# Performance work log

Measured on AMD Instinct MI355X. Metric: run time of the kernel, lower is better.

The kernel has to match this reference:

```python
import jax, jax.numpy as jnp
import numpy as np

D_MODEL = 1024
N_HEADS = 16
D_FF = 4096
EPS = 1e-5


def setup_inputs() -> dict:
    key = jax.random.key(0)
    ks = jax.random.split(key, 13)
    d, f = D_MODEL, D_FF
    s = 1.0 / np.sqrt(d)
    sf = 1.0 / np.sqrt(f)
    return {
        "x": jax.random.normal(ks[0], (2, 2048, d), dtype=jnp.float32),
        "Wq": jax.random.normal(ks[1], (d, d), dtype=jnp.float32) * s,
        "bq": jnp.zeros((d,), jnp.float32),
        "Wk": jax.random.normal(ks[2], (d, d), dtype=jnp.float32) * s,
        "bk": jnp.zeros((d,), jnp.float32),
        "Wv": jax.random.normal(ks[3], (d, d), dtype=jnp.float32) * s,
        "bv": jnp.zeros((d,), jnp.float32),
        "Wo": jax.random.normal(ks[4], (d, d), dtype=jnp.float32) * s,
        "bo": jnp.zeros((d,), jnp.float32),
        "W1": jax.random.normal(ks[5], (f, d), dtype=jnp.float32) * s,
        "b1": jnp.zeros((f,), jnp.float32),
        "W2": jax.random.normal(ks[6], (d, f), dtype=jnp.float32) * sf,
        "b2": jnp.zeros((d,), jnp.float32),
        "g1": jnp.ones((d,), jnp.float32),
        "be1": jnp.zeros((d,), jnp.float32),
        "g2": jnp.ones((d,), jnp.float32),
        "be2": jnp.zeros((d,), jnp.float32),
    }


def _layernorm(x, g, b):
    mu = jnp.mean(x, axis=-1, keepdims=True)
    var = jnp.mean(jnp.square(x - mu), axis=-1, keepdims=True)
    return (x - mu) * jax.lax.rsqrt(var + EPS) * g + b


def reference(x, Wq, bq, Wk, bk, Wv, bv, Wo, bo, W1, b1, W2, b2, g1, be1, g2, be2):
    B, S, D = x.shape
    H = N_HEADS
    dk = D // H
    # QKV projections (torch Linear: x @ W.T + b), reshape to [B,H,S,dk]
    def proj(W, b):
        return (x @ W.T + b).reshape(B, S, H, dk).transpose(0, 2, 1, 3)
    Q, K, V = proj(Wq, bq), proj(Wk, bk), proj(Wv, bv)
    scores = jnp.einsum("bhsd,bhtd->bhst", Q, K) / jnp.sqrt(jnp.float32(dk))
    attn = jax.nn.softmax(scores, axis=-1)
    ctx = jnp.einsum("bhst,bhtd->bhsd", attn, V)
    ctx = ctx.transpose(0, 2, 1, 3).reshape(B, S, D)
    attn_out = ctx @ Wo.T + bo
    x1 = _layernorm(x + attn_out, g1, be1)
    ff = jax.nn.relu(x1 @ W1.T + b1) @ W2.T + b2
    return _layernorm(x1 + ff, g2, be2)
```

## Files before the change

### kernel.cpp

```cpp
#include <hip/hip_runtime.h>

typedef unsigned short u16;
typedef unsigned int u32;
typedef unsigned long long u64;
typedef __attribute__((ext_vector_type(8))) short short8;
typedef __attribute__((ext_vector_type(4))) float f32x4;

#define D_MODEL 1024
#define SEQ 2048
#define NH 16
#define DK 64
#define DFF 4096
#define NTOK 4096
#define LOG2E 1.44269504f

__device__ __forceinline__ u16 f2bf(float f) {
    unsigned x = __builtin_bit_cast(unsigned, f);
    x = x + 0x7fffu + ((x >> 16) & 1u);
    return (u16)(x >> 16);
}

__device__ __forceinline__ float bf2f(u16 v) {
    return __builtin_bit_cast(float, (u32)v << 16);
}

__device__ __forceinline__ float fexp2(float x) {
    float r;
    asm("v_exp_f32 %0, %1" : "=v"(r) : "v"(x));
    return r;
}

__device__ __forceinline__ void gload_lds16(const void* g, void* l) {
    __builtin_amdgcn_global_load_lds(
        (__attribute__((address_space(1))) void*)g,
        (__attribute__((address_space(3))) void*)l, 16, 0, 0);
}

__device__ __forceinline__ void cvt_body(const float* __restrict__ in,
                                         u16* __restrict__ out, int blk) {
    size_t i = ((size_t)blk * 256 + threadIdx.x) * 4;
    float4 v = *(const float4*)(in + i);
    out[i + 0] = f2bf(v.x);
    out[i + 1] = f2bf(v.y);
    out[i + 2] = f2bf(v.z);
    out[i + 3] = f2bf(v.w);
}

__global__ __launch_bounds__(256) void cvt_all(
    const float* __restrict__ sx, const float* __restrict__ s0,
    const float* __restrict__ s1, const float* __restrict__ s2,
    const float* __restrict__ s3, const float* __restrict__ s4,
    const float* __restrict__ s5, u16* __restrict__ dx, u16* __restrict__ d0,
    u16* __restrict__ d1, u16* __restrict__ d2, u16* __restrict__ d3,
    u16* __restrict__ d4, u16* __restrict__ d5) {
    int f = blockIdx.x;
    if (f < 4096) {
        cvt_body(sx, dx, f);
    } else if (f < 8192) {
        int which = (f - 4096) >> 10, blk = (f - 4096) & 1023;
        const float* s = which == 0 ? s0 : which == 1 ? s1 : which == 2 ? s2 : s3;
        u16* d = which == 0 ? d0 : which == 1 ? d1 : which == 2 ? d2 : d3;
        cvt_body(s, d, blk);
    } else if (f < 12288) {
        cvt_body(s4, d4, f - 8192);
    } else {
        cvt_body(s5, d5, f - 12288);
    }
}

template <int BM, int BN>
__device__ __forceinline__ void gemm_acc(const u16* __restrict__ A,
                                         const u16* __restrict__ W,
                                         int K, int m0, int n0,
                                         f32x4 (&acc)[BM / 32][BN / 32]) {
    constexpr int MR = BM / 32, NR = BN / 32;
    __shared__ short8 As[2][BM / 2][8];
    __shared__ short8 Bs[2][BN / 2][8];
    const int tid = threadIdx.x;
    const int lane = tid & 63, w = tid >> 6;
    const int l15 = lane & 15, lg = lane >> 4;
    const int wr = (w >> 1) * (BM / 2), wc = (w & 1) * (BN / 2);
    const int pswA = l15 >> 1;
    const int cbase = ((l15 & 1) << 2) + lg;

#pragma unroll
    for (int i = 0; i < MR; ++i)
#pragma unroll
        for (int j = 0; j < NR; ++j) acc[i][j] = (f32x4){0.f, 0.f, 0.f, 0.f};

#define STAGE_AB(B_, K0)                                                       \
    {                                                                          \
        _Pragma("unroll") for (int j = 0; j < BM / 64; ++j) {                  \
            int idx = j * 256 + tid;                                           \
            int prow = idx >> 3;                                               \
            int s = (idx & 7) ^ (prow & 7);                                    \
            int lrow = prow * 2 + (s >> 2), lc = s & 3;                        \
            gload_lds16(A + (size_t)(m0 + lrow) * K + (K0) + lc * 8,           \
                        (char*)As[B_] + (j * 256 + w * 64) * 16);              \
        }                                                                      \
        _Pragma("unroll") for (int j = 0; j < BN / 64; ++j) {                  \
            int idx = j * 256 + tid;                                           \
            int prow = idx >> 3;                                               \
            int s = (idx & 7) ^ (prow & 7);                                    \
            int lrow = prow * 2 + (s >> 2), lc = s & 3;                        \
            gload_lds16(W + (size_t)(n0 + lrow) * K + (K0) + lc * 8,           \
                        (char*)Bs[B_] + (j * 256 + w * 64) * 16);              \
        }                                                                      \
    }
#define COMPUTE(B_)                                                            \
    {                                                                          \
        short8 af[MR], bf[NR];                                                 \
        _Pragma("unroll") for (int m = 0; m < MR; ++m)                         \
            af[m] = As[B_][(wr + m * 16) / 2 + (l15 >> 1)][cbase ^ pswA];      \
        _Pragma("unroll") for (int n = 0; n < NR; ++n)                         \
            bf[n] = Bs[B_][(wc + n * 16) / 2 + (l15 >> 1)][cbase ^ pswA];      \
        _Pragma("unroll") for (int m = 0; m < MR; ++m)                         \
            _Pragma("unroll") for (int n = 0; n < NR; ++n)                     \
                acc[m][n] = __builtin_amdgcn_mfma_f32_16x16x32_bf16(           \
                    af[m], bf[n], acc[m][n], 0, 0, 0);                         \
    }

    STAGE_AB(0, 0);
    for (int k0 = 0; k0 < K; k0 += 64) {
        __syncthreads();
        STAGE_AB(1, k0 + 32);
        COMPUTE(0);
        __syncthreads();
        if (k0 + 64 < K) STAGE_AB(0, k0 + 64);
        COMPUTE(1);
    }
#undef STAGE_AB
#undef COMPUTE
}

template <int BM, int BN, int EPI, int XCD>
__global__ __launch_bounds__(256) void gemm_bt(
    const u16* __restrict__ A, const u16* __restrict__ W,
    const float* __restrict__ bias, u16* __restrict__ outb,
    float* __restrict__ outf, int M, int N, int K) {
    int m0, n0;
    if (XCD) {
        int f = blockIdx.x;
        int xcd = f & 7, j = f >> 3;
        int mq = xcd >> 1, nh = xcd & 1;
        int mi = j & 7, ni = j >> 3;
        m0 = (mq * 8 + mi) * BM;
        n0 = (nh * 16 + ni) * BN;
    } else {
        m0 = blockIdx.y * BM;
        n0 = blockIdx.x * BN;
    }
    f32x4 acc[BM / 32][BN / 32];
    gemm_acc<BM, BN>(A, W, K, m0, n0, acc);
    const int lane = threadIdx.x & 63, w = threadIdx.x >> 6;
    const int l15 = lane & 15, lg = lane >> 4;
    const int wr = (w >> 1) * (BM / 2), wc = (w & 1) * (BN / 2);
#pragma unroll
    for (int m = 0; m < BM / 32; ++m)
#pragma unroll
        for (int n = 0; n < BN / 32; ++n) {
            int gn = n0 + wc + n * 16 + l15;
            float bv = bias[gn];
#pragma unroll
            for (int r = 0; r < 4; ++r) {
                int gm = m0 + wr + m * 16 + lg * 4 + r;
                float v = acc[m][n][r] + bv;
                if (EPI == 0) outf[(size_t)gm * N + gn] = v;
                else outb[(size_t)gm * N + gn] = f2bf(fmaxf(v, 0.f));
            }
        }
}

__global__ __launch_bounds__(256) void gemm_k64(
    const u16* __restrict__ A, const u16* __restrict__ W,
    const float* __restrict__ bias, u16* __restrict__ outb,
    u16* __restrict__ outb2, int M, int N, int K, int KZ) {
    __shared__ short8 As[64][8];
    __shared__ short8 Bs[128][8];
    const int tid = threadIdx.x;
    const int lane = tid & 63, w = tid >> 6;
    const int l15 = lane & 15, lg = lane >> 4;
    const int wr = (w >> 1) * 32, wc = (w & 1) * 64;
    const int psw = l15 & 7;
    const int f = blockIdx.x;
    const int xcd = f & 7, j = f >> 3;
    const int mi = j & 7, n = (j >> 3) & 7, kz = j >> 6;
    const int m0 = (xcd * 8 + mi) * 64, n0 = n * 128;
    const int kl = K / KZ, kbase = kz * kl;
    u16* out = kz ? outb2 : outb;

    f32x4 acc[2][4];
#pragma unroll
    for (int i = 0; i < 2; ++i)
#pragma unroll
        for (int jj = 0; jj < 4; ++jj) acc[i][jj] = (f32x4){0.f, 0.f, 0.f, 0.f};

    for (int k0 = kbase; k0 < kbase + kl; k0 += 64) {
        __syncthreads();
#pragma unroll
        for (int jj = 0; jj < 2; ++jj) {
            int idx = jj * 256 + tid;
            int r = idx >> 3, ck = idx & 7;
            gload_lds16(A + (size_t)(m0 + r) * K + k0 + ((ck ^ (r & 7)) * 8),
                        (char*)As + (jj * 256 + w * 64) * 16);
        }
#pragma unroll
        for (int jj = 0; jj < 4; ++jj) {
            int idx = jj * 256 + tid;
            int r = idx >> 3, ck = idx & 7;
            gload_lds16(W + (size_t)(n0 + r) * K + k0 + ((ck ^ (r & 7)) * 8),
                        (char*)Bs + (jj * 256 + w * 64) * 16);
        }
        __syncthreads();

#pragma unroll
        for (int kk = 0; kk < 2; ++kk) {
            short8 af[2], bf[4];
#pragma unroll
            for (int m = 0; m < 2; ++m)
                af[m] = As[wr + m * 16 + l15][(kk * 4 + lg) ^ psw];
#pragma unroll
            for (int nn = 0; nn < 4; ++nn)
                bf[nn] = Bs[wc + nn * 16 + l15][(kk * 4 + lg) ^ psw];
#pragma unroll
            for (int m = 0; m < 2; ++m)
#pragma unroll
                for (int nn = 0; nn < 4; ++nn)
                    acc[m][nn] = __builtin_amdgcn_mfma_f32_16x16x32_bf16(
                        af[m], bf[nn], acc[m][nn], 0, 0, 0);
        }
    }

#pragma unroll
    for (int m = 0; m < 2; ++m)
#pragma unroll
        for (int nn = 0; nn < 4; ++nn) {
            int gn = n0 + wc + nn * 16 + l15;
            float bv = (kz == 0) ? bias[gn] : 0.f;
#pragma unroll
            for (int r = 0; r < 4; ++r) {
                int gm = m0 + wr + m * 16 + lg * 4 + r;
                out[(size_t)gm * N + gn] = f2bf(acc[m][nn][r] + bv);
            }
        }
}

__global__ __launch_bounds__(256) void gemm_qkv(
    const u16* __restrict__ A, const u16* __restrict__ Wq,
    const u16* __restrict__ Wk, const u16* __restrict__ Wv,
    const float* __restrict__ bq, const float* __restrict__ bk,
    const float* __restrict__ bv, u16* __restrict__ Qo, u16* __restrict__ Ko,
    u16* __restrict__ Vo) {
    const int f = blockIdx.x;
    const int xcd = f & 7, j = f >> 3;
    const int mi = j & 3, q = j >> 2;
    const int mat = q >> 3;
    const int m0 = (xcd * 4 + mi) * 128, n0 = (q & 7) * 128;
    const u16* W = mat == 0 ? Wq : (mat == 1 ? Wk : Wv);
    const float* bias = mat == 0 ? bq : (mat == 1 ? bk : bv);
    const float scale = (mat == 0) ? 0.125f * LOG2E : 1.0f;
    f32x4 acc[4][4];
    gemm_acc<128, 128>(A, W, D_MODEL, m0, n0, acc);
    const int lane = threadIdx.x & 63, w = threadIdx.x >> 6;
    const int l15 = lane & 15, lg = lane >> 4;
    const int wr = (w >> 1) * 64, wc = (w & 1) * 64;

    if (mat == 2) {
#pragma unroll
        for (int m = 0; m < 4; ++m)
#pragma unroll
            for (int n = 0; n < 4; ++n) {
                int gn = n0 + wc + n * 16 + l15;
                float bv2 = bias[gn];
                int h = gn >> 6, d = gn & 63;
                int gm0 = m0 + wr + m * 16 + lg * 4;
                int b = gm0 >> 11, s = gm0 & 2047;
                u64 pk = (u64)f2bf(acc[m][n][0] + bv2) |
                         ((u64)f2bf(acc[m][n][1] + bv2) << 16) |
                         ((u64)f2bf(acc[m][n][2] + bv2) << 32) |
                         ((u64)f2bf(acc[m][n][3] + bv2) << 48);
                size_t obase = (size_t)(b * NH + h) * DK * SEQ;
                int soff = (s & ~63) + ((((s >> 3) & 7) ^ (d & 7)) << 3) + (s & 7);
                *(u64*)(Vo + obase + (size_t)d * SEQ + soff) = pk;
            }
    } else {
        u16* out = mat == 0 ? Qo : Ko;
#pragma unroll
        for (int m = 0; m < 4; ++m)
#pragma unroll
            for (int n = 0; n < 4; ++n) {
                int gn = n0 + wc + n * 16 + l15;
                float bv2 = bias[gn];
                int h = gn >> 6, d = gn & 63;
#pragma unroll
                for (int r = 0; r < 4; ++r) {
                    int gm = m0 + wr + m * 16 + lg * 4 + r;
                    int b = gm >> 11, s = gm & 2047;
                    float v = (acc[m][n][r] + bv2) * scale;
                    out[(((size_t)(b * NH + h)) * SEQ + s) * DK + d] = f2bf(v);
                }
            }
    }
}

__global__ __launch_bounds__(512) void attn_fwd(const u16* __restrict__ Q,
                                                const u16* __restrict__ Kp,
                                                const u16* __restrict__ Vg_,
                                                u16* __restrict__ ctx) {
    __shared__ __align__(16) u16 Kt[2][128 * 64];
    __shared__ __align__(16) u16 Vt[2][64 * 128];
    __shared__ __align__(16) u16 Ps[8][16 * 64];

    const int tid = threadIdx.x;
    const int lane = tid & 63;
    const int w = tid >> 6;
    const int l15 = lane & 15;
    const int lg = lane >> 4;
    const int f = blockIdx.x + 16 * blockIdx.y;
    const int bh = f & 31;
    const int qblk = f >> 5;
    const int qbase = qblk * 128 + w * 16;
    const u16* Qb = Q + (size_t)bh * SEQ * DK;
    const u16* Kb = Kp + (size_t)bh * SEQ * DK;
    const u16* Vg = Vg_ + (size_t)bh * DK * SEQ;

    short8 qf[2];
#pragma unroll
    for (int hf = 0; hf < 2; ++hf)
        qf[hf] = *(const short8*)(Qb + (size_t)(qbase + l15) * DK + hf * 32 + lg * 8);

    short8 onesf;
#pragma unroll
    for (int e = 0; e < 8; ++e) onesf[e] = (short)0x3F80;

    f32x4 zero = {0.f, 0.f, 0.f, 0.f};
    f32x4 o[4], o1 = zero;
#pragma unroll
    for (int db = 0; db < 4; ++db) o[db] = zero;
    float m_own = 0.f;

    u16* Pu = Ps[w];
    const int psw = l15 & 7;

#define STAGE_V(T0, BUF)                                                       \
    {                                                                          \
        _Pragma("unroll") for (int j = 0; j < 2; ++j) {                        \
            int idx = j * 512 + tid;                                           \
            gload_lds16(Vg + (size_t)(idx >> 4) * SEQ + (T0) + (idx & 15) * 8, \
                        (char*)Vt[BUF] + (j * 512 + w * 64) * 16);             \
        }                                                                      \
    }
#define STAGE_K(T0, BUF)                                                       \
    {                                                                          \
        _Pragma("unroll") for (int j = 0; j < 2; ++j) {                        \
            int idx = j * 512 + tid;                                           \
            int kv = idx >> 3, ck = idx & 7;                                   \
            gload_lds16(Kb + (size_t)((T0) + kv) * DK + ((ck ^ (kv & 7)) * 8), \
                        (char*)Kt[BUF] + (j * 512 + w * 64) * 16);             \
        }                                                                      \
    }
#define KF(BUF, H, NB, HALF)                                                   \
    (*(const short8*)((const char*)Kt[BUF] + ((H)*64 + (NB)*16 + l15) * 128 +  \
                      (((((HALF)*4 + lg)) ^ psw) << 4)))

#define ATTN_TILE(BUF, H)                                                      \
    {                                                                          \
        f32x4 seed = {-m_own, -m_own, -m_own, -m_own};                         \
        f32x4 sc[4];                                                           \
        __builtin_amdgcn_s_setprio(1);                                         \
        _Pragma("unroll") for (int nb = 0; nb < 4; ++nb) {                     \
            sc[nb] = __builtin_amdgcn_mfma_f32_16x16x32_bf16(                  \
                KF(BUF, H, nb, 0), qf[0], seed, 0, 0, 0);                      \
            sc[nb] = __builtin_amdgcn_mfma_f32_16x16x32_bf16(                  \
                KF(BUF, H, nb, 1), qf[1], sc[nb], 0, 0, 0);                    \
        }                                                                      \
        __builtin_amdgcn_s_setprio(0);                                         \
        float a0 = fmaxf(fmaxf(sc[0][0], sc[0][1]), sc[0][2]);                 \
        float a1 = fmaxf(fmaxf(sc[0][3], sc[1][0]), sc[1][1]);                 \
        float a2 = fmaxf(fmaxf(sc[1][2], sc[1][3]), sc[2][0]);                 \
        float a3 = fmaxf(fmaxf(sc[2][1], sc[2][2]), sc[2][3]);                 \
        float a4 = fmaxf(fmaxf(sc[3][0], sc[3][1]), sc[3][2]);                 \
        float lm = fmaxf(fmaxf(fmaxf(a0, a1), a2),                             \
                         fmaxf(fmaxf(a3, a4), sc[3][3]));                      \
        if (__any(lm > 8.f)) {                                                 \
            float rv = fmaxf(lm, __shfl_xor(lm, 16));                          \
            rv = fmaxf(rv, __shfl_xor(rv, 32));                                \
            float rvp = fmaxf(rv, 0.f);                                        \
            float fac = fexp2(-rvp);                                           \
            m_own += rvp;                                                      \
            _Pragma("unroll") for (int nb = 0; nb < 4; ++nb)                   \
                _Pragma("unroll") for (int r = 0; r < 4; ++r)                  \
                    sc[nb][r] -= rvp;                                          \
            _Pragma("unroll") for (int r = 0; r < 4; ++r) {                    \
                float fr = __shfl(fac, lg * 4 + r);                            \
                o1[r] *= fr;                                                   \
                _Pragma("unroll") for (int db = 0; db < 4; ++db)               \
                    o[db][r] *= fr;                                            \
            }                                                                  \
        }                                                                      \
        _Pragma("unroll") for (int nb = 0; nb < 4; ++nb) {                     \
            float p0 = fexp2(sc[nb][0]);                                       \
            float p1 = fexp2(sc[nb][1]);                                       \
            float p2 = fexp2(sc[nb][2]);                                       \
            float p3 = fexp2(sc[nb][3]);                                       \
            u32 pk01 = __builtin_amdgcn_perm(__builtin_bit_cast(u32, p1),      \
                                             __builtin_bit_cast(u32, p0),      \
                                             0x07060302u);                     \
            u32 pk23 = __builtin_amdgcn_perm(__builtin_bit_cast(u32, p3),      \
                                             __builtin_bit_cast(u32, p2),      \
                                             0x07060302u);                     \
            int ck = (nb * 2 + (lg >> 1)) ^ psw;                               \
            u64* dst = (u64*)(Pu + l15 * 64 + ck * 8 + (lg & 1) * 4);          \
            *dst = (u64)pk01 | ((u64)pk23 << 32);                              \
        }                                                                      \
        short8 pa[2];                                                          \
        _Pragma("unroll") for (int ts = 0; ts < 2; ++ts)                       \
            pa[ts] = *(const short8*)(Pu + l15 * 64 + (((ts * 4 + lg) ^ psw) * 8)); \
        __builtin_amdgcn_s_setprio(1);                                         \
        _Pragma("unroll") for (int db = 0; db < 4; ++db) {                     \
            const int d = db * 16 + l15;                                       \
            _Pragma("unroll") for (int ts = 0; ts < 2; ++ts) {                 \
                short8 vb = *(const short8*)((const char*)Vt[BUF] + d * 256 +  \
                                             (((H)*8 + (((ts * 4 + lg) ^ psw))) << 4)); \
                o[db] = __builtin_amdgcn_mfma_f32_16x16x32_bf16(               \
                    pa[ts], vb, o[db], 0, 0, 0);                               \
            }                                                                  \
        }                                                                      \
        o1 = __builtin_amdgcn_mfma_f32_16x16x32_bf16(pa[0], onesf, o1, 0, 0, 0); \
        o1 = __builtin_amdgcn_mfma_f32_16x16x32_bf16(pa[1], onesf, o1, 0, 0, 0); \
        __builtin_amdgcn_s_setprio(0);                                         \
    }

    STAGE_K(0, 0);
    STAGE_V(0, 0);

    for (int t0 = 0; t0 < SEQ; t0 += 256) {
        __syncthreads();
        STAGE_K(t0 + 128, 1);
        STAGE_V(t0 + 128, 1);
        ATTN_TILE(0, 0);
        ATTN_TILE(0, 1);
        __syncthreads();
        if (t0 + 256 < SEQ) {
            STAGE_K(t0 + 256, 0);
            STAGE_V(t0 + 256, 0);
        }
        ATTN_TILE(1, 0);
        ATTN_TILE(1, 1);
    }

    const int b = bh >> 4, h = bh & 15;
#pragma unroll
    for (int r = 0; r < 4; ++r) {
        float inv = 1.0f / o1[r];
        int srow = qbase + lg * 4 + r;
        size_t rowoff = ((size_t)(b * SEQ + srow)) * D_MODEL + h * DK;
#pragma unroll
        for (int db = 0; db < 4; ++db)
            ctx[rowoff + db * 16 + l15] = f2bf(o[db][r] * inv);
    }
#undef STAGE_V
#undef STAGE_K
#undef KF
#undef ATTN_TILE
}

template <bool XBF>
__global__ __launch_bounds__(256) void ln_res(const void* __restrict__ Xv,
                                              const u16* __restrict__ Y,
                                              const u16* __restrict__ Y2,
                                              const float* __restrict__ gamma,
                                              const float* __restrict__ beta,
                                              float* __restrict__ outf,
                                              u16* __restrict__ outb) {
    __shared__ float red[8];
    const int row = blockIdx.x, t = threadIdx.x;
    const size_t off = (size_t)row * D_MODEL + t * 4;
    float x0, x1_, x2, x3;
    if (XBF) {
        ushort4 xv = *(const ushort4*)((const u16*)Xv + off);
        x0 = bf2f(xv.x); x1_ = bf2f(xv.y); x2 = bf2f(xv.z); x3 = bf2f(xv.w);
    } else {
        float4 xv = *(const float4*)((const float*)Xv + off);
        x0 = xv.x; x1_ = xv.y; x2 = xv.z; x3 = xv.w;
    }
    ushort4 yv = *(const ushort4*)(Y + off);
    float sx = x0 + bf2f(yv.x), sy = x1_ + bf2f(yv.y);
    float sz = x2 + bf2f(yv.z), sw = x3 + bf2f(yv.w);
    if (Y2) {
        ushort4 y2 = *(const ushort4*)(Y2 + off);
        sx += bf2f(y2.x); sy += bf2f(y2.y); sz += bf2f(y2.z); sw += bf2f(y2.w);
    }
    float ps = sx + sy + sz + sw;
#pragma unroll
    for (int o2 = 32; o2; o2 >>= 1) ps += __shfl_xor(ps, o2);
    if ((t & 63) == 0) red[t >> 6] = ps;
    __syncthreads();
    float mu = (red[0] + red[1] + red[2] + red[3]) * (1.0f / D_MODEL);
    float d0 = sx - mu, d1 = sy - mu, d2 = sz - mu, d3 = sw - mu;
    float p2 = d0 * d0 + d1 * d1 + d2 * d2 + d3 * d3;
#pragma unroll
    for (int o2 = 32; o2; o2 >>= 1) p2 += __shfl_xor(p2, o2);
    if ((t & 63) == 0) red[4 + (t >> 6)] = p2;
    __syncthreads();
    float var = (red[4] + red[5] + red[6] + red[7]) * (1.0f / D_MODEL);
    float rstd = rsqrtf(var + 1e-5f);
    float4 gv = *(const float4*)(gamma + t * 4);
    float4 bv = *(const float4*)(beta + t * 4);
    float r0 = d0 * rstd * gv.x + bv.x;
    float r1 = d1 * rstd * gv.y + bv.y;
    float r2 = d2 * rstd * gv.z + bv.z;
    float r3 = d3 * rstd * gv.w + bv.w;
    if (outf) {
        float4 res; res.x = r0; res.y = r1; res.z = r2; res.w = r3;
        *(float4*)(outf + off) = res;
    }
    if (outb) {
        outb[off + 0] = f2bf(r0);
        outb[off + 1] = f2bf(r1);
        outb[off + 2] = f2bf(r2);
        outb[off + 3] = f2bf(r3);
    }
}

extern "C" void kernel_launch(void* const* d_in, const int* in_sizes, int n_in,
                              void* d_out, int out_size, void* d_ws, size_t ws_size,
                              hipStream_t stream) {
    (void)in_sizes; (void)n_in; (void)out_size; (void)ws_size;
    const float* x  = (const float*)d_in[0];
    const float* Wq = (const float*)d_in[1];
    const float* bq = (const float*)d_in[2];
    const float* Wk = (const float*)d_in[3];
    const float* bk = (const float*)d_in[4];
    const float* Wv = (const float*)d_in[5];
    const float* bv = (const float*)d_in[6];
    const float* Wo = (const float*)d_in[7];
    const float* bo = (const float*)d_in[8];
    const float* W1 = (const float*)d_in[9];
    const float* b1 = (const float*)d_in[10];
    const float* W2 = (const float*)d_in[11];
    const float* b2 = (const float*)d_in[12];
    const float* g1 = (const float*)d_in[13];
    const float* be1 = (const float*)d_in[14];
    const float* g2 = (const float*)d_in[15];
    const float* be2 = (const float*)d_in[16];

    char* ws = (char*)d_ws;
    u16* xb   = (u16*)(ws);
    u16* Qb   = (u16*)(ws + ((size_t)8 << 20));
    u16* Kb   = (u16*)(ws + ((size_t)16 << 20));
    u16* x1b  = (u16*)(ws + ((size_t)24 << 20));
    u16* W1b  = (u16*)(ws + ((size_t)32 << 20));
    u16* W2b  = (u16*)(ws + ((size_t)40 << 20));
    u16* Fs   = (u16*)(ws + ((size_t)48 << 20));
    u16* Fs2  = (u16*)(ws + ((size_t)56 << 20));
    u16* hb   = (u16*)(ws + ((size_t)64 << 20));
    u16* Wqb = hb;
    u16* Wkb = hb + (1u << 20);
    u16* Wvb = hb + (2u << 20);
    u16* Wob = hb + (3u << 20);
    u16* Vtg = Fs;
    u16* ctxb = xb;

    cvt_all<<<dim3(16384), 256, 0, stream>>>(x, Wq, Wk, Wv, Wo, W1, W2,
                                             xb, Wqb, Wkb, Wvb, Wob, W1b, W2b);

    gemm_qkv<<<dim3(768), 256, 0, stream>>>(xb, Wqb, Wkb, Wvb, bq, bk, bv,
                                            Qb, Kb, Vtg);

    attn_fwd<<<dim3(SEQ / 128, 32), 512, 0, stream>>>(Qb, Kb, Vtg, ctxb);

    gemm_k64<<<dim3(512), 256, 0, stream>>>(ctxb, Wob, bo, Fs, nullptr,
                                            NTOK, D_MODEL, D_MODEL, 1);

    ln_res<false><<<dim3(NTOK), 256, 0, stream>>>(x, Fs, nullptr, g1, be1,
                                                  nullptr, x1b);

    gemm_bt<128, 128, 1, 1><<<dim3(1024), 256, 0, stream>>>(
        x1b, W1b, b1, hb, nullptr, NTOK, DFF, D_MODEL);

    gemm_k64<<<dim3(1024), 256, 0, stream>>>(hb, W2b, b2, Fs, Fs2,
                                             NTOK, D_MODEL, DFF, 2);

    ln_res<true><<<dim3(NTOK), 256, 0, stream>>>(x1b, Fs, Fs2, g2, be2,
                                                 (float*)d_out, nullptr);
}
```

Measured before the change: 254.4 us.

## Switch QKV and FFN1 GEMMs to shared 64x128 single-buffered core

Factors the 64x128 K-step-64 GEMM body out of gemm_k64 into a shared core. The QKV projection and the first FFN GEMM now use it instead of the 128x128 double-buffered gemm_acc path, and the old gemm_bt/gemm_acc code is removed. Grid sizes double to match the smaller tiles. This raises block count and occupancy per GEMM, at the cost of less operand reuse per tile and losing the double-buffered prefetch.

```diff
diff --git a/kernel.cpp b/kernel.cpp
--- a/kernel.cpp
+++ b/kernel.cpp
@@ -68,113 +68,10 @@
     }
 }
 
-template <int BM, int BN>
-__device__ __forceinline__ void gemm_acc(const u16* __restrict__ A,
-                                         const u16* __restrict__ W,
-                                         int K, int m0, int n0,
-                                         f32x4 (&acc)[BM / 32][BN / 32]) {
-    constexpr int MR = BM / 32, NR = BN / 32;
-    __shared__ short8 As[2][BM / 2][8];
-    __shared__ short8 Bs[2][BN / 2][8];
-    const int tid = threadIdx.x;
-    const int lane = tid & 63, w = tid >> 6;
-    const int l15 = lane & 15, lg = lane >> 4;
-    const int wr = (w >> 1) * (BM / 2), wc = (w & 1) * (BN / 2);
-    const int pswA = l15 >> 1;
-    const int cbase = ((l15 & 1) << 2) + lg;
-
-#pragma unroll
-    for (int i = 0; i < MR; ++i)
-#pragma unroll
-        for (int j = 0; j < NR; ++j) acc[i][j] = (f32x4){0.f, 0.f, 0.f, 0.f};
-
-#define STAGE_AB(B_, K0)                                                       \
-    {                                                                          \
-        _Pragma("unroll") for (int j = 0; j < BM / 64; ++j) {                  \
-            int idx = j * 256 + tid;                                           \
-            int prow = idx >> 3;                                               \
-            int s = (idx & 7) ^ (prow & 7);                                    \
-            int lrow = prow * 2 + (s >> 2), lc = s & 3;                        \
-            gload_lds16(A + (size_t)(m0 + lrow) * K + (K0) + lc * 8,           \
-                        (char*)As[B_] + (j * 256 + w * 64) * 16);              \
-        }                                                                      \
-        _Pragma("unroll") for (int j = 0; j < BN / 64; ++j) {                  \
-            int idx = j * 256 + tid;                                           \
-            int prow = idx >> 3;                                               \
-            int s = (idx & 7) ^ (prow & 7);                                    \
-            int lrow = prow * 2 + (s >> 2), lc = s & 3;                        \
-            gload_lds16(W + (size_t)(n0 + lrow) * K + (K0) + lc * 8,           \
-                        (char*)Bs[B_] + (j * 256 + w * 64) * 16);              \
-        }                                                                      \
-    }
-#define COMPUTE(B_)                                                            \
-    {                                                                          \
-        short8 af[MR], bf[NR];                                                 \
-        _Pragma("unroll") for (int m = 0; m < MR; ++m)                         \
-            af[m] = As[B_][(wr + m * 16) / 2 + (l15 >> 1)][cbase ^ pswA];      \
-        _Pragma("unroll") for (int n = 0; n < NR; ++n)                         \
-            bf[n] = Bs[B_][(wc + n * 16) / 2 + (l15 >> 1)][cbase ^ pswA];      \
-        _Pragma("unroll") for (int m = 0; m < MR; ++m)                         \
-            _Pragma("unroll") for (int n = 0; n < NR; ++n)                     \
-                acc[m][n] = __builtin_amdgcn_mfma_f32_16x16x32_bf16(           \
-                    af[m], bf[n], acc[m][n], 0, 0, 0);                         \
-    }
-
-    STAGE_AB(0, 0);
-    for (int k0 = 0; k0 < K; k0 += 64) {
-        __syncthreads();
-        STAGE_AB(1, k0 + 32);
-        COMPUTE(0);
-        __syncthreads();
-        if (k0 + 64 < K) STAGE_AB(0, k0 + 64);
-        COMPUTE(1);
-    }
-#undef STAGE_AB
-#undef COMPUTE
-}
-
-template <int BM, int BN, int EPI, int XCD>
-__global__ __launch_bounds__(256) void gemm_bt(
-    const u16* __restrict__ A, const u16* __restrict__ W,
-    const float* __restrict__ bias, u16* __restrict__ outb,
-    float* __restrict__ outf, int M, int N, int K) {
-    int m0, n0;
-    if (XCD) {
-        int f = blockIdx.x;
-        int xcd = f & 7, j = f >> 3;
-        int mq = xcd >> 1, nh = xcd & 1;
-        int mi = j & 7, ni = j >> 3;
-        m0 = (mq * 8 + mi) * BM;
-        n0 = (nh * 16 + ni) * BN;
-    } else {
-        m0 = blockIdx.y * BM;
-        n0 = blockIdx.x * BN;
-    }
-    f32x4 acc[BM / 32][BN / 32];
-    gemm_acc<BM, BN>(A, W, K, m0, n0, acc);
-    const int lane = threadIdx.x & 63, w = threadIdx.x >> 6;
-    const int l15 = lane & 15, lg = lane >> 4;
-    const int wr = (w >> 1) * (BM / 2), wc = (w & 1) * (BN / 2);
-#pragma unroll
-    for (int m = 0; m < BM / 32; ++m)
-#pragma unroll
-        for (int n = 0; n < BN / 32; ++n) {
-            int gn = n0 + wc + n * 16 + l15;
-            float bv = bias[gn];
-#pragma unroll
-            for (int r = 0; r < 4; ++r) {
-                int gm = m0 + wr + m * 16 + lg * 4 + r;
-                float v = acc[m][n][r] + bv;
-                if (EPI == 0) outf[(size_t)gm * N + gn] = v;
-                else outb[(size_t)gm * N + gn] = f2bf(fmaxf(v, 0.f));
-            }
-        }
-}
-
-__global__ __launch_bounds__(256) void gemm_k64(
-    const u16* __restrict__ A, const u16* __restrict__ W,
-    const float* __restrict__ bias, u16* __restrict__ outb,
-    u16* __restrict__ outb2, int M, int N, int K, int KZ) {
+__device__ __forceinline__ void gemm_core64(const u16* __restrict__ A,
+                                            const u16* __restrict__ W, int K,
+                                            int m0, int n0, int kbase, int kl,
+                                            f32x4 (&acc)[2][4]) {
     __shared__ short8 As[64][8];
     __shared__ short8 Bs[128][8];
     const int tid = threadIdx.x;
@@ -182,14 +79,7 @@
     const int l15 = lane & 15, lg = lane >> 4;
     const int wr = (w >> 1) * 32, wc = (w & 1) * 64;
     const int psw = l15 & 7;
-    const int f = blockIdx.x;
-    const int xcd = f & 7, j = f >> 3;
-    const int mi = j & 7, n = (j >> 3) & 7, kz = j >> 6;
-    const int m0 = (xcd * 8 + mi) * 64, n0 = n * 128;
-    const int kl = K / KZ, kbase = kz * kl;
-    u16* out = kz ? outb2 : outb;
-
-    f32x4 acc[2][4];
+
 #pragma unroll
     for (int i = 0; i < 2; ++i)
 #pragma unroll
@@ -230,7 +120,25 @@
                         af[m], bf[nn], acc[m][nn], 0, 0, 0);
         }
     }
-
+}
+
+__global__ __launch_bounds__(256) void gemm_k64(
+    const u16* __restrict__ A, const u16* __restrict__ W,
+    const float* __restrict__ bias, u16* __restrict__ outb,
+    u16* __restrict__ outb2, int M, int N, int K, int KZ) {
+    const int f = blockIdx.x;
+    const int xcd = f & 7, j = f >> 3;
+    const int mi = j & 7, n = (j >> 3) & 7, kz = j >> 6;
+    const int m0 = (xcd * 8 + mi) * 64, n0 = n * 128;
+    const int kl = K / KZ, kbase = kz * kl;
+    u16* out = kz ? outb2 : outb;
+
+    f32x4 acc[2][4];
+    gemm_core64(A, W, K, m0, n0, kbase, kl, acc);
+
+    const int lane = threadIdx.x & 63, w = threadIdx.x >> 6;
+    const int l15 = lane & 15, lg = lane >> 4;
+    const int wr = (w >> 1) * 32, wc = (w & 1) * 64;
 #pragma unroll
     for (int m = 0; m < 2; ++m)
 #pragma unroll
@@ -241,6 +149,35 @@
             for (int r = 0; r < 4; ++r) {
                 int gm = m0 + wr + m * 16 + lg * 4 + r;
                 out[(size_t)gm * N + gn] = f2bf(acc[m][nn][r] + bv);
+            }
+        }
+}
+
+__global__ __launch_bounds__(256) void gemm_k64_relu(
+    const u16* __restrict__ A, const u16* __restrict__ W,
+    const float* __restrict__ bias, u16* __restrict__ outb, int M, int N,
+    int K) {
+    const int f = blockIdx.x;
+    const int xcd = f & 7, j = f >> 3;
+    const int mi = j & 7, n = j >> 3;
+    const int m0 = (xcd * 8 + mi) * 64, n0 = n * 128;
+
+    f32x4 acc[2][4];
+    gemm_core64(A, W, K, m0, n0, 0, K, acc);
+
+    const int lane = threadIdx.x & 63, w = threadIdx.x >> 6;
+    const int l15 = lane & 15, lg = lane >> 4;
+    const int wr = (w >> 1) * 32, wc = (w & 1) * 64;
+#pragma unroll
+    for (int m = 0; m < 2; ++m)
+#pragma unroll
+        for (int nn = 0; nn < 4; ++nn) {
+            int gn = n0 + wc + nn * 16 + l15;
+            float bv = bias[gn];
+#pragma unroll
+            for (int r = 0; r < 4; ++r) {
+                int gm = m0 + wr + m * 16 + lg * 4 + r;
+                outb[(size_t)gm * N + gn] = f2bf(fmaxf(acc[m][nn][r] + bv, 0.f));
             }
         }
 }
@@ -253,32 +190,34 @@
     u16* __restrict__ Vo) {
     const int f = blockIdx.x;
     const int xcd = f & 7, j = f >> 3;
-    const int mi = j & 3, q = j >> 2;
+    const int mi = j & 7, q = j >> 3;
     const int mat = q >> 3;
-    const int m0 = (xcd * 4 + mi) * 128, n0 = (q & 7) * 128;
+    const int m0 = (xcd * 8 + mi) * 64, n0 = (q & 7) * 128;
     const u16* W = mat == 0 ? Wq : (mat == 1 ? Wk : Wv);
     const float* bias = mat == 0 ? bq : (mat == 1 ? bk : bv);
     const float scale = (mat == 0) ? 0.125f * LOG2E : 1.0f;
-    f32x4 acc[4][4];
-    gemm_acc<128, 128>(A, W, D_MODEL, m0, n0, acc);
+
+    f32x4 acc[2][4];
+    gemm_core64(A, W, D_MODEL, m0, n0, 0, D_MODEL, acc);
+
     const int lane = threadIdx.x & 63, w = threadIdx.x >> 6;
     const int l15 = lane & 15, lg = lane >> 4;
-    const int wr = (w >> 1) * 64, wc = (w & 1) * 64;
+    const int wr = (w >> 1) * 32, wc = (w & 1) * 64;
 
     if (mat == 2) {
 #pragma unroll
-        for (int m = 0; m < 4; ++m)
-#pragma unroll
-            for (int n = 0; n < 4; ++n) {
-                int gn = n0 + wc + n * 16 + l15;
+        for (int m = 0; m < 2; ++m)
+#pragma unroll
+            for (int nn = 0; nn < 4; ++nn) {
+                int gn = n0 + wc + nn * 16 + l15;
                 float bv2 = bias[gn];
                 int h = gn >> 6, d = gn & 63;
                 int gm0 = m0 + wr + m * 16 + lg * 4;
                 int b = gm0 >> 11, s = gm0 & 2047;
-                u64 pk = (u64)f2bf(acc[m][n][0] + bv2) |
-                         ((u64)f2bf(acc[m][n][1] + bv2) << 16) |
-                         ((u64)f2bf(acc[m][n][2] + bv2) << 32) |
-                         ((u64)f2bf(acc[m][n][3] + bv2) << 48);
+                u64 pk = (u64)f2bf(acc[m][nn][0] + bv2) |
+                         ((u64)f2bf(acc[m][nn][1] + bv2) << 16) |
+                         ((u64)f2bf(acc[m][nn][2] + bv2) << 32) |
+                         ((u64)f2bf(acc[m][nn][3] + bv2) << 48);
                 size_t obase = (size_t)(b * NH + h) * DK * SEQ;
                 int soff = (s & ~63) + ((((s >> 3) & 7) ^ (d & 7)) << 3) + (s & 7);
                 *(u64*)(Vo + obase + (size_t)d * SEQ + soff) = pk;
@@ -286,17 +225,17 @@
     } else {
         u16* out = mat == 0 ? Qo : Ko;
 #pragma unroll
-        for (int m = 0; m < 4; ++m)
-#pragma unroll
-            for (int n = 0; n < 4; ++n) {
-                int gn = n0 + wc + n * 16 + l15;
+        for (int m = 0; m < 2; ++m)
+#pragma unroll
+            for (int nn = 0; nn < 4; ++nn) {
+                int gn = n0 + wc + nn * 16 + l15;
                 float bv2 = bias[gn];
                 int h = gn >> 6, d = gn & 63;
 #pragma unroll
                 for (int r = 0; r < 4; ++r) {
                     int gm = m0 + wr + m * 16 + lg * 4 + r;
                     int b = gm >> 11, s = gm & 2047;
-                    float v = (acc[m][n][r] + bv2) * scale;
+                    float v = (acc[m][nn][r] + bv2) * scale;
                     out[(((size_t)(b * NH + h)) * SEQ + s) * DK + d] = f2bf(v);
                 }
             }
@@ -565,8 +504,8 @@
     cvt_all<<<dim3(16384), 256, 0, stream>>>(x, Wq, Wk, Wv, Wo, W1, W2,
                                              xb, Wqb, Wkb, Wvb, Wob, W1b, W2b);
 
-    gemm_qkv<<<dim3(768), 256, 0, stream>>>(xb, Wqb, Wkb, Wvb, bq, bk, bv,
-                                            Qb, Kb, Vtg);
+    gemm_qkv<<<dim3(1536), 256, 0, stream>>>(xb, Wqb, Wkb, Wvb, bq, bk, bv,
+                                             Qb, Kb, Vtg);
 
     attn_fwd<<<dim3(SEQ / 128, 32), 512, 0, stream>>>(Qb, Kb, Vtg, ctxb);
 
@@ -576,8 +515,8 @@
     ln_res<false><<<dim3(NTOK), 256, 0, stream>>>(x, Fs, nullptr, g1, be1,
                                                   nullptr, x1b);
 
-    gemm_bt<128, 128, 1, 1><<<dim3(1024), 256, 0, stream>>>(
-        x1b, W1b, b1, hb, nullptr, NTOK, DFF, D_MODEL);
+    gemm_k64_relu<<<dim3(2048), 256, 0, stream>>>(x1b, W1b, b1, hb,
+                                                  NTOK, DFF, D_MODEL);
 
     gemm_k64<<<dim3(1024), 256, 0, stream>>>(hb, W2b, b2, Fs, Fs2,
                                              NTOK, D_MODEL, DFF, 2);
```

Measured after the change: 227.8 us. 1.12x faster.
